# Kernel optimization log

Measured on AMD Instinct MI355X. Metric: run time of the kernel, lower is better.

The kernel has to match this reference:

```python
import jax, jax.numpy as jnp
import numpy as np

B, T, C, H = 8, 2048, 1024, 128

def setup_inputs() -> dict:
    key = jax.random.key(0)
    k1, k2, k3, k4 = jax.random.split(key, 4)
    s = 1.0 / np.sqrt(C)
    return {
        "x": jax.random.normal(k1, (B, T, C), dtype=jnp.float32),
        "Wq": jax.random.normal(k2, (C, H), dtype=jnp.float32) * s,
        "Wk": jax.random.normal(k3, (C, H), dtype=jnp.float32) * s,
        "Wv": jax.random.normal(k4, (C, H), dtype=jnp.float32) * s,
    }

def reference(x, Wq, Wk, Wv):
    # q,k,v: [B,T,H]
    q = jnp.einsum('btc,ch->bth', x, Wq)
    k = jnp.einsum('btc,ch->bth', x, Wk)
    v = jnp.einsum('btc,ch->bth', x, Wv)
    scale = k.shape[-1] ** -0.5
    wei = jnp.einsum('bqh,bkh->bqk', q, k) * scale  # [B,T,T]
    # NOTE: original forward never applies the tril mask -> full bidirectional softmax
    wei = jax.nn.softmax(wei, axis=-1)
    # dropout p=0 (eval): identity
    out = jnp.einsum('bqk,bkh->bqh', wei, v)  # [B,T,H]
    return out
```

## Files before the change

### kernel.cpp

```cpp
#include <hip/hip_runtime.h>

typedef __attribute__((ext_vector_type(4))) float  f32x4;
typedef __attribute__((ext_vector_type(8))) short  s16x8;
typedef __attribute__((ext_vector_type(4))) unsigned int u32x4;
typedef __attribute__((ext_vector_type(4))) unsigned short u16x4;

#define NB 8
#define NT 2048
#define NC 1024
#define NH 128
#define NM (NB * NT)

__device__ __forceinline__ unsigned short f2bf(float f) {
  union { float f; unsigned u; } v; v.f = f;
  unsigned r = v.u + 0x7FFFu + ((v.u >> 16) & 1u);
  return (unsigned short)(r >> 16);
}
__device__ __forceinline__ unsigned pack2(float a, float b) {
  return (unsigned)f2bf(a) | ((unsigned)f2bf(b) << 16);
}
__device__ __forceinline__ f32x4 mfma16(s16x8 a, s16x8 b, f32x4 c) {
  return __builtin_amdgcn_mfma_f32_16x16x32_bf16(a, b, c, 0, 0, 0);
}

__global__ __launch_bounds__(256) void k_prep_w(
    const float* __restrict__ wq, const float* __restrict__ wk,
    const float* __restrict__ wv, unsigned short* __restrict__ wt3) {
  __shared__ float ts[64][65];
  const int tid = threadIdx.x;
  const int w = blockIdx.x >> 5;
  const int rem = blockIdx.x & 31;
  const int c0 = (rem >> 1) * 64;
  const int h0 = (rem & 1) * 64;
  const float* W = (w == 0) ? wq : (w == 1) ? wk : wv;
  const int hl = tid & 63, ci = tid >> 6;
  #pragma unroll
  for (int i = 0; i < 16; ++i) {
    int cl = i * 4 + ci;
    ts[cl][hl] = W[(size_t)(c0 + cl) * NH + h0 + hl];
  }
  __syncthreads();
  const int cl2 = tid & 63, hi2 = tid >> 6;
  #pragma unroll
  for (int j = 0; j < 16; ++j) {
    int hl2 = j * 4 + hi2;
    float v = ts[cl2][hl2];
    if (w == 0) v *= 0.08838834764831845f;
    wt3[(size_t)w * 131072 + (size_t)(h0 + hl2) * NC + c0 + cl2] = f2bf(v);
  }
}

__global__ __launch_bounds__(512, 2) void k_qkv(
    const float* __restrict__ x, const unsigned short* __restrict__ wt3,
    unsigned short* __restrict__ qo, unsigned short* __restrict__ ko,
    unsigned short* __restrict__ vo) {
  __shared__ u32x4 xs4[32768 / 16];
  char* xs = (char*)xs4;
  const int tid = threadIdx.x;
  const int lane = tid & 63;
  const int w = tid >> 6;
  const int mg = w >> 2;
  const int ng = w & 3;
  const int m0 = blockIdx.x * 128;
  const int n0 = blockIdx.y * 192 + ng * 48;
  const int c15 = lane & 15;
  const int g4 = lane >> 4;

  const int sr = tid >> 2;
  const float* xp = x + (size_t)(m0 + sr) * NC + (tid & 3) * 16;
  const int wbA = (sr * 128 + (tid & 3) * 32) ^ ((sr & 7) << 4);
  const int wbB = (sr * 128 + (tid & 3) * 32 + 16) ^ ((sr & 7) << 4);

  f32x4 acc[4][3] = {};
  f32x4 xr[4];
  #pragma unroll
  for (int j = 0; j < 4; ++j) xr[j] = *(const f32x4*)(xp + j * 4);
  auto pack_write = [&](int buf) {
    u32x4 gA = { pack2(xr[0].x, xr[0].y), pack2(xr[0].z, xr[0].w),
                 pack2(xr[1].x, xr[1].y), pack2(xr[1].z, xr[1].w) };
    u32x4 gB = { pack2(xr[2].x, xr[2].y), pack2(xr[2].z, xr[2].w),
                 pack2(xr[3].x, xr[3].y), pack2(xr[3].z, xr[3].w) };
    *(u32x4*)(xs + buf * 16384 + wbA) = gA;
    *(u32x4*)(xs + buf * 16384 + wbB) = gB;
  };
  pack_write(0);
  __syncthreads();

  const int aswz = (c15 & 7) << 4;
  for (int kt = 0; kt < 16; ++kt) {
    if (kt < 15) {
      #pragma unroll
      for (int j = 0; j < 4; ++j) xr[j] = *(const f32x4*)(xp + (kt + 1) * 64 + j * 4);
    }
    s16x8 wf[2][3];
    {
      const unsigned short* wpb = wt3 + (size_t)(n0 + c15) * NC + kt * 64 + g4 * 8;
      #pragma unroll
      for (int ks = 0; ks < 2; ++ks)
        #pragma unroll
        for (int nj = 0; nj < 3; ++nj)
          wf[ks][nj] = *(const s16x8*)(wpb + (size_t)nj * 16 * NC + ks * 32);
    }
    char* cb = xs + (kt & 1) * 16384;
    #pragma unroll
    for (int ks = 0; ks < 2; ++ks) {
      #pragma unroll
      for (int mf = 0; mf < 4; ++mf) {
        int arow = mg * 64 + mf * 16 + c15;
        s16x8 af = *(const s16x8*)(cb + ((arow * 128 + ks * 64 + g4 * 16) ^ aswz));
        #pragma unroll
        for (int nj = 0; nj < 3; ++nj)
          acc[mf][nj] = mfma16(af, wf[ks][nj], acc[mf][nj]);
      }
    }
    if (kt < 15) pack_write((kt + 1) & 1);
    __syncthreads();
  }
  #pragma unroll
  for (int mf = 0; mf < 4; ++mf) {
    #pragma unroll
    for (int nj = 0; nj < 3; ++nj) {
      f32x4 a = acc[mf][nj];
      int gcol = n0 + nj * 16 + c15;
      int gr = m0 + mg * 64 + mf * 16 + g4 * 4;
      int h = gcol & 127;
      if (gcol < 256) {
        unsigned short* dst = (gcol < 128) ? qo : ko;
        dst[(size_t)(gr + 0) * NH + h] = f2bf(a.x);
        dst[(size_t)(gr + 1) * NH + h] = f2bf(a.y);
        dst[(size_t)(gr + 2) * NH + h] = f2bf(a.z);
        dst[(size_t)(gr + 3) * NH + h] = f2bf(a.w);
      } else {
        int bb = gr >> 11, tt = gr & 2047;
        u16x4 pv = { f2bf(a.x), f2bf(a.y), f2bf(a.z), f2bf(a.w) };
        *(u16x4*)(vo + ((size_t)(bb * NH + h) * NT + tt)) = pv;
      }
    }
  }
}

__global__ __launch_bounds__(512, 2) void k_attn(
    const unsigned short* __restrict__ qg, const unsigned short* __restrict__ kg,
    const unsigned short* __restrict__ vg, float* __restrict__ out) {
  __shared__ u32x4 lds4[147456 / 16];
  char* L = (char*)lds4;
  const int tid = threadIdx.x;
  const int lane = tid & 63;
  const int w = tid >> 6;
  const int grp = w & 1;
  const int qs = w >> 1;
  const int gl = qs * 64 + lane;
  const int b = blockIdx.y;
  const int qr0 = blockIdx.x * 64;
  const int c15 = lane & 15;
  const int g4 = lane >> 4;
  const int kv0 = grp * 1024;

  char* Kg = L + grp * 65536;
  char* Vg = Kg + 32768;
  char* pw = L + 131072 + w * 2048;

  s16x8 qf[4];
  #pragma unroll
  for (int ks = 0; ks < 4; ++ks)
    qf[ks] = *(const s16x8*)(qg + (size_t)(b * NT + qr0 + qs * 16 + c15) * NH + ks * 32 + g4 * 8);

  float m_run[4], lsum[4];
  #pragma unroll
  for (int r = 0; r < 4; ++r) { m_run[r] = -3.0e38f; lsum[r] = 0.0f; }
  f32x4 acc_o[8] = {};

  const int srow = gl >> 4;
  const unsigned short* kptr = kg + (size_t)(b * NT + kv0 + srow) * NH + (gl & 15) * 8;
  const unsigned short* vptr = vg + (size_t)(b * NH + srow) * NT + kv0 + (gl & 15) * 8;

  u32x4 kreg[8], vreg[8];
  auto stage = [&](int kt) {
    #pragma unroll
    for (int i = 0; i < 8; ++i) {
      kreg[i] = *(const u32x4*)(kptr + ((size_t)(kt * 128 + i * 16)) * NH);
      vreg[i] = *(const u32x4*)(vptr + (size_t)(i * 16) * NT + kt * 128);
    }
  };
  auto write_tiles = [&]() {
    #pragma unroll
    for (int i = 0; i < 8; ++i) {
      int r = srow + i * 16;
      int off = (r * 256 + (gl & 15) * 16) ^ ((r & 7) << 4);
      *(u32x4*)(Kg + off) = kreg[i];
      *(u32x4*)(Vg + off) = vreg[i];
    }
  };
  stage(0);
  write_tiles();
  __syncthreads();

  for (int kt = 0; kt < 8; ++kt) {
    if (kt < 7) stage(kt + 1);
    f32x4 s[8];
    __builtin_amdgcn_s_setprio(1);
    #pragma unroll
    for (int nj = 0; nj < 8; ++nj) {
      f32x4 acc_s = {};
      int kr = nj * 16 + c15;
      int kswz = (kr & 7) << 4;
      #pragma unroll
      for (int ks = 0; ks < 4; ++ks) {
        s16x8 bf = *(const s16x8*)(Kg + ((kr * 256 + ks * 64 + g4 * 16) ^ kswz));
        acc_s = mfma16(qf[ks], bf, acc_s);
      }
      s[nj] = acc_s;
    }
    __builtin_amdgcn_s_setprio(0);
    float alpha[4];
    #pragma unroll
    for (int r = 0; r < 4; ++r) {
      float pm = fmaxf(fmaxf(fmaxf(s[0][r], s[1][r]), fmaxf(s[2][r], s[3][r])),
                       fmaxf(fmaxf(s[4][r], s[5][r]), fmaxf(s[6][r], s[7][r])));
      pm = fmaxf(pm, __shfl_xor(pm, 1));
      pm = fmaxf(pm, __shfl_xor(pm, 2));
      pm = fmaxf(pm, __shfl_xor(pm, 4));
      pm = fmaxf(pm, __shfl_xor(pm, 8));
      float mn = fmaxf(m_run[r], pm);
      alpha[r] = __expf(m_run[r] - mn);
      m_run[r] = mn;
      float psum = 0.0f;
      #pragma unroll
      for (int nj = 0; nj < 8; ++nj) {
        float e = __expf(s[nj][r] - mn);
        s[nj][r] = e;
        psum += e;
      }
      lsum[r] = lsum[r] * alpha[r] + psum;
    }
    #pragma unroll
    for (int hj = 0; hj < 8; ++hj) {
      acc_o[hj][0] *= alpha[0]; acc_o[hj][1] *= alpha[1];
      acc_o[hj][2] *= alpha[2]; acc_o[hj][3] *= alpha[3];
    }
    #pragma unroll
    for (int half = 0; half < 2; ++half) {
      #pragma unroll
      for (int nj = 0; nj < 4; ++nj) {
        #pragma unroll
        for (int r = 0; r < 4; ++r) {
          int row = g4 * 4 + r;
          *(unsigned short*)(pw + ((row * 128 + (nj * 16 + c15) * 2) ^ ((row & 7) << 4)))
              = f2bf(s[half * 4 + nj][r]);
        }
      }
      __builtin_amdgcn_s_setprio(1);
      #pragma unroll
      for (int ks2 = 0; ks2 < 2; ++ks2) {
        s16x8 pa = *(const s16x8*)(pw + ((c15 * 128 + ks2 * 64 + g4 * 16) ^ ((c15 & 7) << 4)));
        int vcb = (half * 2 + ks2) * 64 + g4 * 16;
        #pragma unroll
        for (int hj = 0; hj < 8; ++hj) {
          int vr = hj * 16 + c15;
          s16x8 bv = *(const s16x8*)(Vg + ((vr * 256 + vcb) ^ ((vr & 7) << 4)));
          acc_o[hj] = mfma16(pa, bv, acc_o[hj]);
        }
      }
      __builtin_amdgcn_s_setprio(0);
    }
    __syncthreads();
    if (kt < 7) write_tiles();
    __syncthreads();
  }
  float l_run[4];
  #pragma unroll
  for (int r = 0; r < 4; ++r) {
    float ls = lsum[r];
    ls += __shfl_xor(ls, 1);
    ls += __shfl_xor(ls, 2);
    ls += __shfl_xor(ls, 4);
    ls += __shfl_xor(ls, 8);
    l_run[r] = ls;
  }
  float* msh = (float*)(L + 131072);
  float* lsh = msh + 64;
  if (grp == 1) {
    #pragma unroll
    for (int r = 0; r < 4; ++r) {
      int row = qs * 16 + g4 * 4 + r;
      #pragma unroll
      for (int hj = 0; hj < 8; ++hj)
        *(float*)(L + row * 512 + (hj * 16 + c15) * 4) = acc_o[hj][r];
      if (c15 == 0) { msh[row] = m_run[r]; lsh[row] = l_run[r]; }
    }
  }
  __syncthreads();
  if (grp == 0) {
    #pragma unroll
    for (int r = 0; r < 4; ++r) {
      int row = qs * 16 + g4 * 4 + r;
      float m1 = msh[row], l1 = lsh[row];
      float M = fmaxf(m_run[r], m1);
      float w0 = __expf(m_run[r] - M);
      float w1 = __expf(m1 - M);
      float den = 1.0f / (w0 * l_run[r] + w1 * l1);
      #pragma unroll
      for (int hj = 0; hj < 8; ++hj) {
        float o1 = *(const float*)(L + row * 512 + (hj * 16 + c15) * 4);
        out[(size_t)(b * NT + qr0 + row) * NH + hj * 16 + c15] =
            (w0 * acc_o[hj][r] + w1 * o1) * den;
      }
    }
  }
}

extern "C" void kernel_launch(void* const* d_in, const int* in_sizes, int n_in,
                              void* d_out, int out_size, void* d_ws, size_t ws_size,
                              hipStream_t stream) {
  const float* x  = (const float*)d_in[0];
  const float* wq = (const float*)d_in[1];
  const float* wk = (const float*)d_in[2];
  const float* wv = (const float*)d_in[3];
  unsigned short* ws  = (unsigned short*)d_ws;
  unsigned short* qb  = ws;
  unsigned short* kb  = ws + (size_t)2 * 1024 * 1024;
  unsigned short* vb  = ws + (size_t)4 * 1024 * 1024;
  unsigned short* wt3 = ws + (size_t)6 * 1024 * 1024;

  k_prep_w<<<dim3(96), dim3(256), 0, stream>>>(wq, wk, wv, wt3);
  k_qkv<<<dim3(128, 2), dim3(512), 0, stream>>>(x, wt3, qb, kb, vb);
  k_attn<<<dim3(NT / 64, NB), dim3(512), 0, stream>>>(qb, kb, vb, (float*)d_out);
}
```

Baseline: 184.0 us.

## Halve QKV projection M-tile and prefetch x two steps ahead

The QKV projection kernel now uses 64-row M tiles instead of 128, doubling the grid to 512 blocks and raising launch bounds to 4 blocks per CU with half the LDS. The x loads are restructured so each thread loads 8 floats per step, prefetched two k-steps ahead into alternating register buffers before packing to bf16 LDS. The aim is more parallelism across the MI355X's CUs and better hiding of global-load latency. The cost is that each B fragment of the weights is reused over fewer rows, so weight traffic per output doubles.

```diff
diff --git a/kernel.cpp b/kernel.cpp
--- a/kernel.cpp
+++ b/kernel.cpp
@@ -50,47 +50,43 @@
   }
 }
 
-__global__ __launch_bounds__(512, 2) void k_qkv(
+__global__ __launch_bounds__(512, 4) void k_qkv(
     const float* __restrict__ x, const unsigned short* __restrict__ wt3,
     unsigned short* __restrict__ qo, unsigned short* __restrict__ ko,
     unsigned short* __restrict__ vo) {
-  __shared__ u32x4 xs4[32768 / 16];
+  __shared__ u32x4 xs4[16384 / 16];
   char* xs = (char*)xs4;
   const int tid = threadIdx.x;
   const int lane = tid & 63;
   const int w = tid >> 6;
   const int mg = w >> 2;
   const int ng = w & 3;
-  const int m0 = blockIdx.x * 128;
+  const int m0 = blockIdx.x * 64;
   const int n0 = blockIdx.y * 192 + ng * 48;
   const int c15 = lane & 15;
   const int g4 = lane >> 4;
 
-  const int sr = tid >> 2;
-  const float* xp = x + (size_t)(m0 + sr) * NC + (tid & 3) * 16;
-  const int wbA = (sr * 128 + (tid & 3) * 32) ^ ((sr & 7) << 4);
-  const int wbB = (sr * 128 + (tid & 3) * 32 + 16) ^ ((sr & 7) << 4);
-
-  f32x4 acc[4][3] = {};
-  f32x4 xr[4];
-  #pragma unroll
-  for (int j = 0; j < 4; ++j) xr[j] = *(const f32x4*)(xp + j * 4);
-  auto pack_write = [&](int buf) {
-    u32x4 gA = { pack2(xr[0].x, xr[0].y), pack2(xr[0].z, xr[0].w),
-                 pack2(xr[1].x, xr[1].y), pack2(xr[1].z, xr[1].w) };
-    u32x4 gB = { pack2(xr[2].x, xr[2].y), pack2(xr[2].z, xr[2].w),
-                 pack2(xr[3].x, xr[3].y), pack2(xr[3].z, xr[3].w) };
-    *(u32x4*)(xs + buf * 16384 + wbA) = gA;
-    *(u32x4*)(xs + buf * 16384 + wbB) = gB;
-  };
-  pack_write(0);
+  const int sr = tid >> 3;
+  const float* xp = x + (size_t)(m0 + sr) * NC + (tid & 7) * 8;
+  const int wb = (sr * 128 + (tid & 7) * 16) ^ ((sr & 7) << 4);
+
+  f32x4 acc[2][3] = {};
+  f32x4 xA[2], xB[2];
+  xA[0] = *(const f32x4*)(xp);          xA[1] = *(const f32x4*)(xp + 4);
+  xB[0] = *(const f32x4*)(xp + 64);     xB[1] = *(const f32x4*)(xp + 68);
+  {
+    u32x4 pk = { pack2(xA[0].x, xA[0].y), pack2(xA[0].z, xA[0].w),
+                 pack2(xA[1].x, xA[1].y), pack2(xA[1].z, xA[1].w) };
+    *(u32x4*)(xs + wb) = pk;
+  }
   __syncthreads();
 
   const int aswz = (c15 & 7) << 4;
   for (int kt = 0; kt < 16; ++kt) {
-    if (kt < 15) {
-      #pragma unroll
-      for (int j = 0; j < 4; ++j) xr[j] = *(const f32x4*)(xp + (kt + 1) * 64 + j * 4);
+    if (kt + 2 < 16) {
+      f32x4* dst = (kt & 1) ? xB : xA;
+      dst[0] = *(const f32x4*)(xp + (kt + 2) * 64);
+      dst[1] = *(const f32x4*)(xp + (kt + 2) * 64 + 4);
     }
     s16x8 wf[2][3];
     {
@@ -101,28 +97,33 @@
         for (int nj = 0; nj < 3; ++nj)
           wf[ks][nj] = *(const s16x8*)(wpb + (size_t)nj * 16 * NC + ks * 32);
     }
-    char* cb = xs + (kt & 1) * 16384;
+    char* cb = xs + (kt & 1) * 8192;
     #pragma unroll
     for (int ks = 0; ks < 2; ++ks) {
       #pragma unroll
-      for (int mf = 0; mf < 4; ++mf) {
-        int arow = mg * 64 + mf * 16 + c15;
+      for (int mf = 0; mf < 2; ++mf) {
+        int arow = mg * 32 + mf * 16 + c15;
         s16x8 af = *(const s16x8*)(cb + ((arow * 128 + ks * 64 + g4 * 16) ^ aswz));
         #pragma unroll
         for (int nj = 0; nj < 3; ++nj)
           acc[mf][nj] = mfma16(af, wf[ks][nj], acc[mf][nj]);
       }
     }
-    if (kt < 15) pack_write((kt + 1) & 1);
+    if (kt + 1 < 16) {
+      f32x4* srcp = ((kt + 1) & 1) ? xB : xA;
+      u32x4 pk = { pack2(srcp[0].x, srcp[0].y), pack2(srcp[0].z, srcp[0].w),
+                   pack2(srcp[1].x, srcp[1].y), pack2(srcp[1].z, srcp[1].w) };
+      *(u32x4*)(xs + ((kt + 1) & 1) * 8192 + wb) = pk;
+    }
     __syncthreads();
   }
   #pragma unroll
-  for (int mf = 0; mf < 4; ++mf) {
+  for (int mf = 0; mf < 2; ++mf) {
     #pragma unroll
     for (int nj = 0; nj < 3; ++nj) {
       f32x4 a = acc[mf][nj];
       int gcol = n0 + nj * 16 + c15;
-      int gr = m0 + mg * 64 + mf * 16 + g4 * 4;
+      int gr = m0 + mg * 32 + mf * 16 + g4 * 4;
       int h = gcol & 127;
       if (gcol < 256) {
         unsigned short* dst = (gcol < 128) ? qo : ko;
@@ -323,6 +324,6 @@
   unsigned short* wt3 = ws + (size_t)6 * 1024 * 1024;
 
   k_prep_w<<<dim3(96), dim3(256), 0, stream>>>(wq, wk, wv, wt3);
-  k_qkv<<<dim3(128, 2), dim3(512), 0, stream>>>(x, wt3, qb, kb, vb);
+  k_qkv<<<dim3(256, 2), dim3(512), 0, stream>>>(x, wt3, qb, kb, vb);
   k_attn<<<dim3(NT / 64, NB), dim3(512), 0, stream>>>(qb, kb, vb, (float*)d_out);
 }
```

After: 188.1 us. 2.2% more time.
